# Optimization experiments

Measured on AMD Instinct MI355X. Metric: run time of the kernel, lower is better.

The kernel has to match this reference:

```python
import jax, jax.numpy as jnp
import numpy as np
import math

B, S, E, H = 8, 1024, 1024, 16
HD = E // H  # 64


def setup_inputs() -> dict:
    key = jax.random.key(0)
    ks = jax.random.split(key, 13)
    scale = 1.0 / math.sqrt(E)
    inp = {
        "query": jax.random.normal(ks[0], (B, S, E), jnp.float32),
        "key": jax.random.normal(ks[1], (B, S, E), jnp.float32),
        "value": jax.random.normal(ks[2], (B, S, E), jnp.float32),
        "mask": jax.random.randint(ks[3], (B, S, S), 0, 2, jnp.int32),
        "adjoin_matrix": jax.random.normal(ks[4], (B, S, S), jnp.float32),
        "Wq": jax.random.uniform(ks[5], (E, E), jnp.float32, -scale, scale),
        "bq": jax.random.uniform(ks[6], (E,), jnp.float32, -scale, scale),
        "Wk": jax.random.uniform(ks[7], (E, E), jnp.float32, -scale, scale),
        "bk": jax.random.uniform(ks[8], (E,), jnp.float32, -scale, scale),
        "Wv": jax.random.uniform(ks[9], (E, E), jnp.float32, -scale, scale),
        "bv": jax.random.uniform(ks[10], (E,), jnp.float32, -scale, scale),
        "Wo": jax.random.uniform(ks[11], (E, E), jnp.float32, -scale, scale),
        "bo": jax.random.uniform(ks[12], (E,), jnp.float32, -scale, scale),
    }
    return inp


def reference(query, key, value, mask, adjoin_matrix, Wq, bq, Wk, bk, Wv, bv, Wo, bo):
    def split_heads(x):
        # [B,S,E] -> [B,H,S,HD]
        return x.reshape(B, S, H, HD).transpose(0, 2, 1, 3)

    q = split_heads(query @ Wq.T + bq)
    k = split_heads(key @ Wk.T + bk)
    v = split_heads(value @ Wv.T + bv)

    # scaled logits: [B,H,S,S]
    logits = jnp.einsum("bhqd,bhkd->bhqk", q, k) / jnp.sqrt(jnp.asarray(HD, q.dtype))
    # additive mask (broadcast over heads)
    logits = logits + mask[:, None, :, :].astype(logits.dtype) * (-1e9)
    attn = jax.nn.softmax(logits, axis=-1)
    # post-softmax adjoin-matrix addition
    attn = attn + adjoin_matrix[:, None, :, :]

    x = jnp.einsum("bhqk,bhkd->bhqd", attn, v)  # [B,H,S,HD]
    x = x.transpose(0, 2, 1, 3).reshape(B, S, E)
    out = x @ Wo.T + bo
    return out, attn
```

## Files before the change

### kernel.cpp

```cpp
#include <hip/hip_runtime.h>
#include <stdint.h>

#define BB 8
#define SS 1024
#define EE 1024
#define HH 16
#define HDD 64

typedef unsigned short u16_t;
typedef __attribute__((ext_vector_type(8))) short short8;
typedef __attribute__((ext_vector_type(4))) float f32x4;

__device__ __forceinline__ u16_t f2bf(float f){
    union { float f; uint32_t u; } v; v.f = f;
    return (u16_t)((v.u + 0x7fffu + ((v.u >> 16) & 1u)) >> 16);
}
__device__ __forceinline__ float bf2f(u16_t u){
    union { uint32_t u; float f; } v; v.u = ((uint32_t)u) << 16;
    return v.f;
}

__device__ __forceinline__ void gload_lds16(const void* g, void* l){
    __builtin_amdgcn_global_load_lds((const __attribute__((address_space(1))) unsigned int*)g,
                                     (__attribute__((address_space(3))) unsigned int*)l, 16, 0, 0);
}

#define MFMA16(a,b,c) __builtin_amdgcn_mfma_f32_16x16x32_bf16(a,b,c,0,0,0)

union U8 { short8 v; u16_t u[8]; };

__global__ __launch_bounds__(256) void cvt3_f32_bf16(const float* __restrict__ s0,
                                                     const float* __restrict__ s1,
                                                     const float* __restrict__ s2,
                                                     u16_t* __restrict__ d0,
                                                     u16_t* __restrict__ d1,
                                                     u16_t* __restrict__ d2, int n8){
    const float* in = (blockIdx.z == 0) ? s0 : (blockIdx.z == 1 ? s1 : s2);
    u16_t* out      = (blockIdx.z == 0) ? d0 : (blockIdx.z == 1 ? d1 : d2);
    int i = blockIdx.x * blockDim.x + threadIdx.x;
    int stride = gridDim.x * blockDim.x;
    for (; i < n8; i += stride){
        const float4* p = (const float4*)(in + (size_t)i * 8);
        float4 a = p[0], b = p[1];
        U8 o;
        o.u[0]=f2bf(a.x); o.u[1]=f2bf(a.y); o.u[2]=f2bf(a.z); o.u[3]=f2bf(a.w);
        o.u[4]=f2bf(b.x); o.u[5]=f2bf(b.y); o.u[6]=f2bf(b.z); o.u[7]=f2bf(b.w);
        *(short8*)(out + (size_t)i * 8) = o.v;
    }
}

__global__ __launch_bounds__(256) void cvtW4_f32_bf16(const float* __restrict__ s0,
                                                      const float* __restrict__ s1,
                                                      const float* __restrict__ s2,
                                                      const float* __restrict__ s3,
                                                      u16_t* __restrict__ d0,
                                                      u16_t* __restrict__ d1,
                                                      u16_t* __restrict__ d2,
                                                      u16_t* __restrict__ d3, int n8){
    const float* in;
    u16_t* out;
    switch (blockIdx.z){
        case 0: in = s0; out = d0; break;
        case 1: in = s1; out = d1; break;
        case 2: in = s2; out = d2; break;
        default: in = s3; out = d3; break;
    }
    int i = blockIdx.x * blockDim.x + threadIdx.x;
    int stride = gridDim.x * blockDim.x;
    for (; i < n8; i += stride){
        const float4* p = (const float4*)(in + (size_t)i * 8);
        float4 a = p[0], b = p[1];
        U8 o;
        o.u[0]=f2bf(a.x); o.u[1]=f2bf(a.y); o.u[2]=f2bf(a.z); o.u[3]=f2bf(a.w);
        o.u[4]=f2bf(b.x); o.u[5]=f2bf(b.y); o.u[6]=f2bf(b.z); o.u[7]=f2bf(b.w);
        *(short8*)(out + (size_t)i * 8) = o.v;
    }
}

__global__ __launch_bounds__(256) void cvt_mask(const int* __restrict__ mask,
                                                u16_t* __restrict__ mb, int n8){
    int i = blockIdx.x * blockDim.x + threadIdx.x;
    int stride = gridDim.x * blockDim.x;
    for (; i < n8; i += stride){
        const int4* p = (const int4*)(mask + (size_t)i * 8);
        int4 a = p[0], b = p[1];
        U8 o;
        o.u[0]=a.x?0xCE6Eu:0u; o.u[1]=a.y?0xCE6Eu:0u; o.u[2]=a.z?0xCE6Eu:0u; o.u[3]=a.w?0xCE6Eu:0u;
        o.u[4]=b.x?0xCE6Eu:0u; o.u[5]=b.y?0xCE6Eu:0u; o.u[6]=b.z?0xCE6Eu:0u; o.u[7]=b.w?0xCE6Eu:0u;
        *(short8*)(mb + (size_t)i * 8) = o.v;
    }
}

__global__ __launch_bounds__(256) void transpose_v(const u16_t* __restrict__ Vp,
                                                   u16_t* __restrict__ Vt){
    __shared__ u16_t sT[64 * 66];
    const int b = blockIdx.z, h = blockIdx.y, s0 = blockIdx.x * 64;
    const int tid = threadIdx.x;
    #pragma unroll
    for (int it = 0; it < 2; it++){
        int c = it * 256 + tid;
        int sr = c >> 3, c8 = c & 7;
        short8 v = *(const short8*)(Vp + (size_t)(b * SS + s0 + sr) * EE + h * HDD + c8 * 8);
        *(short8*)(sT + sr * 66 + c8 * 8) = v;
    }
    __syncthreads();
    #pragma unroll
    for (int it = 0; it < 2; it++){
        int c = it * 256 + tid;
        int dr = c >> 3, c8 = c & 7;
        U8 o;
        #pragma unroll
        for (int e = 0; e < 8; e++) o.u[e] = sT[(c8 * 8 + e) * 66 + dr];
        *(short8*)(Vt + ((size_t)(b * HH + h) * HDD + dr) * SS + s0 + c8 * 8) = o.v;
    }
}

__device__ __forceinline__ void xcd_tiles(int& m0, int& n0){
    int i = blockIdx.x + blockIdx.y * 8;
    int k = i & 7, q = i >> 3;
    m0 = (k * 8 + (q >> 3)) * 128;
    n0 = (q & 7) * 128;
}

__global__ __launch_bounds__(256) void gemm_bt3(const u16_t* __restrict__ qb,
                                                const u16_t* __restrict__ kb,
                                                const u16_t* __restrict__ vb,
                                                const u16_t* __restrict__ Wqb,
                                                const u16_t* __restrict__ Wkb,
                                                const u16_t* __restrict__ Wvb,
                                                const float* __restrict__ bq,
                                                const float* __restrict__ bk,
                                                const float* __restrict__ bv,
                                                u16_t* __restrict__ Qp,
                                                u16_t* __restrict__ Kp,
                                                u16_t* __restrict__ Vp)
{
    const u16_t *A, *Bw; const float* bias; u16_t* Cout;
    switch (blockIdx.z){
        case 0:  A = qb; Bw = Wqb; bias = bq; Cout = Qp; break;
        case 1:  A = kb; Bw = Wkb; bias = bk; Cout = Kp; break;
        default: A = vb; Bw = Wvb; bias = bv; Cout = Vp; break;
    }
    const int K = EE, N = EE;

    __shared__ u16_t sA[128 * 32];
    __shared__ u16_t sB[128 * 32];
    const int tid = threadIdx.x;
    const int wave = tid >> 6, lane = tid & 63;
    int m0, n0; xcd_tiles(m0, n0);
    const int wm = (wave >> 1) * 64, wn = (wave & 1) * 64;

    f32x4 acc[4][4] = {};

    for (int k0 = 0; k0 < K; k0 += 32){
        #pragma unroll
        for (int i = 0; i < 2; i++){
            int s   = (wave * 2 + i) * 64 + lane;
            int row = s >> 2, cb = (s & 3) * 8;
            gload_lds16(A  + (size_t)(m0 + row) * K + k0 + cb, (void*)(sA + (wave * 2 + i) * 512));
            gload_lds16(Bw + (size_t)(n0 + row) * K + k0 + cb, (void*)(sB + (wave * 2 + i) * 512));
        }
        __syncthreads();

        short8 aF[4], bF[4];
        #pragma unroll
        for (int m = 0; m < 4; m++)
            aF[m] = *(const short8*)(sA + (wm + m * 16 + (lane & 15)) * 32 + (lane >> 4) * 8);
        #pragma unroll
        for (int n = 0; n < 4; n++)
            bF[n] = *(const short8*)(sB + (wn + n * 16 + (lane & 15)) * 32 + (lane >> 4) * 8);
        #pragma unroll
        for (int m = 0; m < 4; m++)
            #pragma unroll
            for (int n = 0; n < 4; n++)
                acc[m][n] = MFMA16(aF[m], bF[n], acc[m][n]);
        __syncthreads();
    }

    #pragma unroll
    for (int m = 0; m < 4; m++){
        #pragma unroll
        for (int n = 0; n < 4; n++){
            int col = n0 + wn + n * 16 + (lane & 15);
            float bvv = bias[col];
            #pragma unroll
            for (int j = 0; j < 4; j++){
                int row = m0 + wm + m * 16 + (lane >> 4) * 4 + j;
                Cout[(size_t)row * N + col] = f2bf(acc[m][n][j] + bvv);
            }
        }
    }
}

__global__ __launch_bounds__(256) void gemm_bt_f32(const u16_t* __restrict__ A,
                                                   const u16_t* __restrict__ Bw,
                                                   const float* __restrict__ bias,
                                                   float* __restrict__ Cout,
                                                   int M, int N, int K)
{
    __shared__ u16_t sA[128 * 32];
    __shared__ u16_t sB[128 * 32];
    const int tid = threadIdx.x;
    const int wave = tid >> 6, lane = tid & 63;
    int m0, n0; xcd_tiles(m0, n0);
    const int wm = (wave >> 1) * 64, wn = (wave & 1) * 64;

    f32x4 acc[4][4] = {};

    for (int k0 = 0; k0 < K; k0 += 32){
        #pragma unroll
        for (int i = 0; i < 2; i++){
            int s   = (wave * 2 + i) * 64 + lane;
            int row = s >> 2, cb = (s & 3) * 8;
            gload_lds16(A  + (size_t)(m0 + row) * K + k0 + cb, (void*)(sA + (wave * 2 + i) * 512));
            gload_lds16(Bw + (size_t)(n0 + row) * K + k0 + cb, (void*)(sB + (wave * 2 + i) * 512));
        }
        __syncthreads();

        short8 aF[4], bF[4];
        #pragma unroll
        for (int m = 0; m < 4; m++)
            aF[m] = *(const short8*)(sA + (wm + m * 16 + (lane & 15)) * 32 + (lane >> 4) * 8);
        #pragma unroll
        for (int n = 0; n < 4; n++)
            bF[n] = *(const short8*)(sB + (wn + n * 16 + (lane & 15)) * 32 + (lane >> 4) * 8);
        #pragma unroll
        for (int m = 0; m < 4; m++)
            #pragma unroll
            for (int n = 0; n < 4; n++)
                acc[m][n] = MFMA16(aF[m], bF[n], acc[m][n]);
        __syncthreads();
    }

    #pragma unroll
    for (int m = 0; m < 4; m++){
        #pragma unroll
        for (int n = 0; n < 4; n++){
            int col = n0 + wn + n * 16 + (lane & 15);
            float bv = bias[col];
            #pragma unroll
            for (int j = 0; j < 4; j++){
                int row = m0 + wm + m * 16 + (lane >> 4) * 4 + j;
                Cout[(size_t)row * N + col] = acc[m][n][j] + bv;
            }
        }
    }
}

__global__ __launch_bounds__(256, 3) void attn_fused(const u16_t* __restrict__ Qp,
                                                     const u16_t* __restrict__ Kp,
                                                     const u16_t* __restrict__ Vt,
                                                     const u16_t* __restrict__ maskb,
                                                     const float* __restrict__ adjoin,
                                                     float* __restrict__ attn,
                                                     u16_t* __restrict__ X)
{
    __shared__ u16_t sL[16384];
    u16_t* sVT = sL + 8192;
    u16_t* sPB = sL + 12288;

    const int flat = blockIdx.x;
    const int b  = flat & 7;
    const int i0 = ((flat >> 3) & 15) * 64;
    const int h  = flat >> 7;
    const int tid = threadIdx.x, wave = tid >> 6, lane = tid & 63;
    const int frow = lane & 15, fks = lane >> 4;
    const int bh = b * HH + h;

    #pragma unroll
    for (int i = 0; i < 2; i++){
        int chunk = (wave * 2 + i) * 64 + lane;
        int row = chunk >> 3, slot = chunk & 7;
        gload_lds16(Qp + (size_t)(b * SS + i0 + row) * EE + h * HDD + (slot ^ (row & 7)) * 8,
                    (void*)(sPB + (wave * 2 + i) * 512));
    }
    __syncthreads();
    short8 aQ0, aQ1;
    {
        int row = wave * 16 + frow;
        aQ0 = *(const short8*)((const char*)sPB + row * 128 + ((fks * 16)      ^ ((row & 7) << 4)));
        aQ1 = *(const short8*)((const char*)sPB + row * 128 + ((64 + fks * 16) ^ ((row & 7) << 4)));
    }
    __syncthreads();

    auto stageK64 = [&](int j0, u16_t* dst){
        #pragma unroll
        for (int i = 0; i < 2; i++){
            int chunk = (wave * 2 + i) * 64 + lane;
            int row = chunk >> 3, slot = chunk & 7;
            gload_lds16(Kp + (size_t)(b * SS + j0 + row) * EE + h * HDD + (slot ^ (row & 7)) * 8,
                        (void*)(dst + (wave * 2 + i) * 512));
        }
    };
    auto stageK128 = [&](int j0, u16_t* dst){
        #pragma unroll
        for (int i = 0; i < 4; i++){
            int chunk = (wave * 4 + i) * 64 + lane;
            int row = chunk >> 3, slot = chunk & 7;
            gload_lds16(Kp + (size_t)(b * SS + j0 + row) * EE + h * HDD + (slot ^ (row & 7)) * 8,
                        (void*)(dst + (wave * 4 + i) * 512));
        }
    };
    auto stageVT = [&](int j0){
        #pragma unroll
        for (int i = 0; i < 2; i++){
            int chunk = (wave * 2 + i) * 64 + lane;
            int row = chunk >> 3, slot = chunk & 7;
            gload_lds16(Vt + ((size_t)bh * HDD + row) * SS + j0 + (slot ^ (row & 7)) * 8,
                        (void*)(sVT + (wave * 2 + i) * 512));
        }
    };

    const int grow0 = i0 + wave * 16 + fks * 4;
    const size_t mrowbase = (size_t)(b * SS + grow0) * SS;

    float s_run[4] = {0.f, 0.f, 0.f, 0.f};
    {
        u16_t* bufs[2] = { sL, sL + 8192 };
        stageK128(0, bufs[0]);
        #pragma unroll
        for (int T = 0; T < 8; T++){
            u16_t* cur = bufs[T & 1];
            __syncthreads();
            if (T < 7) stageK128((T + 1) * 128, bufs[(T + 1) & 1]);
            #pragma unroll
            for (int half = 0; half < 2; half++){
                const int t64 = T * 128 + half * 64;
                float mbv[4][4];
                #pragma unroll
                for (int n = 0; n < 4; n++)
                    #pragma unroll
                    for (int r = 0; r < 4; r++)
                        mbv[n][r] = bf2f(maskb[mrowbase + (size_t)r * SS + t64 + n * 16 + frow]);
                __builtin_amdgcn_s_setprio(1);
                #pragma unroll
                for (int n = 0; n < 4; n++){
                    int jrow = half * 64 + n * 16 + frow;
                    f32x4 acc = {};
                    short8 bF = *(const short8*)((const char*)cur + jrow * 128 + ((fks * 16)      ^ ((jrow & 7) << 4)));
                    acc = MFMA16(aQ0, bF, acc);
                    bF        = *(const short8*)((const char*)cur + jrow * 128 + ((64 + fks * 16) ^ ((jrow & 7) << 4)));
                    acc = MFMA16(aQ1, bF, acc);
                    #pragma unroll
                    for (int r = 0; r < 4; r++)
                        s_run[r] += __expf(acc[r] * 0.125f + mbv[n][r]);
                }
                __builtin_amdgcn_s_setprio(0);
            }
        }
    }
    float inv[4];
    #pragma unroll
    for (int r = 0; r < 4; r++){
        float v = s_run[r];
        v += __shfl_xor(v, 1); v += __shfl_xor(v, 2); v += __shfl_xor(v, 4); v += __shfl_xor(v, 8);
        inv[r] = 1.0f / v;
    }

    f32x4 accPV[4] = {};
    __syncthreads();
    u16_t* sK2[2] = { sL, sL + 4096 };
    stageK64(0, sK2[0]);
    #pragma unroll
    for (int t = 0; t < 16; t++){
        const int cur = t & 1;
        __syncthreads();
        if (t < 15) stageK64((t + 1) * 64, sK2[cur ^ 1]);
        stageVT(t * 64);
        float mbv[4][4], adjv[4][4];
        #pragma unroll
        for (int n = 0; n < 4; n++)
            #pragma unroll
            for (int r = 0; r < 4; r++){
                size_t off = mrowbase + (size_t)r * SS + t * 64 + n * 16 + frow;
                mbv[n][r]  = bf2f(maskb[off]);
                adjv[n][r] = adjoin[off];
            }
        __builtin_amdgcn_s_setprio(1);
        #pragma unroll
        for (int n = 0; n < 4; n++){
            int jrow = n * 16 + frow;
            f32x4 acc = {};
            short8 bF = *(const short8*)((const char*)sK2[cur] + jrow * 128 + ((fks * 16)      ^ ((jrow & 7) << 4)));
            acc = MFMA16(aQ0, bF, acc);
            bF        = *(const short8*)((const char*)sK2[cur] + jrow * 128 + ((64 + fks * 16) ^ ((jrow & 7) << 4)));
            acc = MFMA16(aQ1, bF, acc);
            #pragma unroll
            for (int r = 0; r < 4; r++){
                int irow = wave * 16 + fks * 4 + r;
                float att = __expf(acc[r] * 0.125f + mbv[n][r]) * inv[r] + adjv[n][r];
                *(u16_t*)((char*)sPB + irow * 128 + (((n * 16 + frow) * 2) ^ ((irow & 7) << 4))) = f2bf(att);
            }
        }
        __builtin_amdgcn_s_setprio(0);
        __syncthreads();
        __builtin_amdgcn_s_setprio(1);
        {
            int prow = wave * 16 + frow;
            short8 aP0 = *(const short8*)((const char*)sPB + prow * 128 + ((fks * 16)      ^ ((prow & 7) << 4)));
            short8 aP1 = *(const short8*)((const char*)sPB + prow * 128 + ((64 + fks * 16) ^ ((prow & 7) << 4)));
            #pragma unroll
            for (int n = 0; n < 4; n++){
                int drow = n * 16 + frow;
                short8 bV0 = *(const short8*)((const char*)sVT + drow * 128 + ((fks * 16)      ^ ((drow & 7) << 4)));
                short8 bV1 = *(const short8*)((const char*)sVT + drow * 128 + ((64 + fks * 16) ^ ((drow & 7) << 4)));
                accPV[n] = MFMA16(aP0, bV0, accPV[n]);
                accPV[n] = MFMA16(aP1, bV1, accPV[n]);
            }
        }
        __builtin_amdgcn_s_setprio(0);
        {
            int rr = tid >> 4, c4 = tid & 15;
            #pragma unroll
            for (int it = 0; it < 4; it++){
                int row = it * 16 + rr;
                uint2 pv = *(const uint2*)((const char*)sPB + row * 128 + ((c4 * 8) ^ ((row & 7) << 4)));
                float4 o;
                o.x = bf2f((u16_t)(pv.x & 0xffffu));
                o.y = bf2f((u16_t)(pv.x >> 16));
                o.z = bf2f((u16_t)(pv.y & 0xffffu));
                o.w = bf2f((u16_t)(pv.y >> 16));
                *(float4*)(attn + ((size_t)bh * SS + i0 + row) * SS + t * 64 + c4 * 4) = o;
            }
        }
    }

    #pragma unroll
    for (int n = 0; n < 4; n++){
        #pragma unroll
        for (int j = 0; j < 4; j++){
            int row = i0 + wave * 16 + fks * 4 + j;
            int col = h * HDD + n * 16 + frow;
            X[(size_t)(b * SS + row) * EE + col] = f2bf(accPV[n][j]);
        }
    }
}

extern "C" void kernel_launch(void* const* d_in, const int* in_sizes, int n_in,
                              void* d_out, int out_size, void* d_ws, size_t ws_size,
                              hipStream_t stream)
{
    const float* query  = (const float*)d_in[0];
    const float* key    = (const float*)d_in[1];
    const float* value  = (const float*)d_in[2];
    const int*   mask   = (const int*)  d_in[3];
    const float* adjoin = (const float*)d_in[4];
    const float* Wq = (const float*)d_in[5];
    const float* bq = (const float*)d_in[6];
    const float* Wk = (const float*)d_in[7];
    const float* bk = (const float*)d_in[8];
    const float* Wv = (const float*)d_in[9];
    const float* bv = (const float*)d_in[10];
    const float* Wo = (const float*)d_in[11];
    const float* bo = (const float*)d_in[12];

    float* out  = (float*)d_out;
    float* attn = out + (size_t)BB * SS * EE;

    const size_t nBSE = (size_t)BB * SS * EE;
    const size_t nEE  = (size_t)EE * EE;

    u16_t* p  = (u16_t*)d_ws;
    u16_t* qb  = p; p += nBSE;
    u16_t* kb  = p; p += nBSE;
    u16_t* vb  = p; p += nBSE;
    u16_t* Qp  = p; p += nBSE;
    u16_t* Kp  = p; p += nBSE;
    u16_t* Vp  = p; p += nBSE;
    u16_t* Xa  = p; p += nBSE;
    u16_t* Wqb = p; p += nEE;
    u16_t* Wkb = p; p += nEE;
    u16_t* Wvb = p; p += nEE;
    u16_t* Wob = p; p += nEE;

    u16_t* Vt    = qb;
    u16_t* maskb = kb;

    cvt3_f32_bf16<<<dim3(1024, 1, 3), 256, 0, stream>>>(query, key, value, qb, kb, vb, (int)(nBSE / 8));
    cvtW4_f32_bf16<<<dim3(256, 1, 4), 256, 0, stream>>>(Wq, Wk, Wv, Wo, Wqb, Wkb, Wvb, Wob, (int)(nEE / 8));

    dim3 gProj(EE / 128, (BB * SS) / 128);
    gemm_bt3<<<dim3(EE / 128, (BB * SS) / 128, 3), 256, 0, stream>>>(qb, kb, vb, Wqb, Wkb, Wvb,
                                                                     bq, bk, bv, Qp, Kp, Vp);

    dim3 gT(SS / 64, HH, BB);
    transpose_v<<<gT, 256, 0, stream>>>(Vp, Vt);
    cvt_mask<<<1024, 256, 0, stream>>>(mask, maskb, (int)(nBSE / 8));

    attn_fused<<<2048, 256, 0, stream>>>(Qp, Kp, Vt, maskb, adjoin, attn, Xa);

    gemm_bt_f32<<<gProj, 256, 0, stream>>>(Xa, Wob, bo, out, BB * SS, EE, EE);
}
```

Measured before the change: 406.7 us.

## Process 128 keys per barrier pair in attention second pass

Restructures the second attention pass so each iteration handles two 64-key halves, with separate K, V-transpose and probability buffers for each half. This halves the number of block-wide barriers and loop iterations, amortising synchronisation cost. K is no longer double-buffered across iterations; the next K tile is issued after the barrier instead of prefetched earlier. Shared memory grows from 32KB to 48KB, which may limit occupancy at the declared 3 blocks per CU.

```diff
diff --git a/kernel.cpp b/kernel.cpp
--- a/kernel.cpp
+++ b/kernel.cpp
@@ -255,9 +255,13 @@
                                                      float* __restrict__ attn,
                                                      u16_t* __restrict__ X)
 {
-    __shared__ u16_t sL[16384];
-    u16_t* sVT = sL + 8192;
-    u16_t* sPB = sL + 12288;
+    __shared__ u16_t sL[24576];
+    u16_t* sK0  = sL;
+    u16_t* sK1  = sL + 4096;
+    u16_t* sVT0 = sL + 8192;
+    u16_t* sVT1 = sL + 12288;
+    u16_t* sPB0 = sL + 16384;
+    u16_t* sPB1 = sL + 20480;
 
     const int flat = blockIdx.x;
     const int b  = flat & 7;
@@ -272,14 +276,14 @@
         int chunk = (wave * 2 + i) * 64 + lane;
         int row = chunk >> 3, slot = chunk & 7;
         gload_lds16(Qp + (size_t)(b * SS + i0 + row) * EE + h * HDD + (slot ^ (row & 7)) * 8,
-                    (void*)(sPB + (wave * 2 + i) * 512));
+                    (void*)(sPB0 + (wave * 2 + i) * 512));
     }
     __syncthreads();
     short8 aQ0, aQ1;
     {
         int row = wave * 16 + frow;
-        aQ0 = *(const short8*)((const char*)sPB + row * 128 + ((fks * 16)      ^ ((row & 7) << 4)));
-        aQ1 = *(const short8*)((const char*)sPB + row * 128 + ((64 + fks * 16) ^ ((row & 7) << 4)));
+        aQ0 = *(const short8*)((const char*)sPB0 + row * 128 + ((fks * 16)      ^ ((row & 7) << 4)));
+        aQ1 = *(const short8*)((const char*)sPB0 + row * 128 + ((64 + fks * 16) ^ ((row & 7) << 4)));
     }
     __syncthreads();
 
@@ -301,13 +305,13 @@
                         (void*)(dst + (wave * 4 + i) * 512));
         }
     };
-    auto stageVT = [&](int j0){
+    auto stageVT64 = [&](int j0, u16_t* dst){
         #pragma unroll
         for (int i = 0; i < 2; i++){
             int chunk = (wave * 2 + i) * 64 + lane;
             int row = chunk >> 3, slot = chunk & 7;
             gload_lds16(Vt + ((size_t)bh * HDD + row) * SS + j0 + (slot ^ (row & 7)) * 8,
-                        (void*)(sVT + (wave * 2 + i) * 512));
+                        (void*)(dst + (wave * 2 + i) * 512));
         }
     };
 
@@ -359,68 +363,78 @@
 
     f32x4 accPV[4] = {};
     __syncthreads();
-    u16_t* sK2[2] = { sL, sL + 4096 };
-    stageK64(0, sK2[0]);
-    #pragma unroll
-    for (int t = 0; t < 16; t++){
-        const int cur = t & 1;
+    stageK64(0, sK0); stageK64(64, sK1);
+    #pragma unroll
+    for (int T = 0; T < 8; T++){
         __syncthreads();
-        if (t < 15) stageK64((t + 1) * 64, sK2[cur ^ 1]);
-        stageVT(t * 64);
-        float mbv[4][4], adjv[4][4];
-        #pragma unroll
-        for (int n = 0; n < 4; n++)
-            #pragma unroll
-            for (int r = 0; r < 4; r++){
-                size_t off = mrowbase + (size_t)r * SS + t * 64 + n * 16 + frow;
-                mbv[n][r]  = bf2f(maskb[off]);
-                adjv[n][r] = adjoin[off];
+        stageVT64(T * 128, sVT0);
+        stageVT64(T * 128 + 64, sVT1);
+        #pragma unroll
+        for (int half = 0; half < 2; half++){
+            const u16_t* sKh = half ? sK1 : sK0;
+            u16_t* sPh = half ? sPB1 : sPB0;
+            const int t64 = T * 128 + half * 64;
+            float mbv[4][4], adjv[4][4];
+            #pragma unroll
+            for (int n = 0; n < 4; n++)
+                #pragma unroll
+                for (int r = 0; r < 4; r++){
+                    size_t off = mrowbase + (size_t)r * SS + t64 + n * 16 + frow;
+                    mbv[n][r]  = bf2f(maskb[off]);
+                    adjv[n][r] = adjoin[off];
+                }
+            __builtin_amdgcn_s_setprio(1);
+            #pragma unroll
+            for (int n = 0; n < 4; n++){
+                int jrow = n * 16 + frow;
+                f32x4 acc = {};
+                short8 bF = *(const short8*)((const char*)sKh + jrow * 128 + ((fks * 16)      ^ ((jrow & 7) << 4)));
+                acc = MFMA16(aQ0, bF, acc);
+                bF        = *(const short8*)((const char*)sKh + jrow * 128 + ((64 + fks * 16) ^ ((jrow & 7) << 4)));
+                acc = MFMA16(aQ1, bF, acc);
+                #pragma unroll
+                for (int r = 0; r < 4; r++){
+                    int irow = wave * 16 + fks * 4 + r;
+                    float att = __expf(acc[r] * 0.125f + mbv[n][r]) * inv[r] + adjv[n][r];
+                    *(u16_t*)((char*)sPh + irow * 128 + (((n * 16 + frow) * 2) ^ ((irow & 7) << 4))) = f2bf(att);
+                }
             }
+            __builtin_amdgcn_s_setprio(0);
+        }
+        __syncthreads();
+        if (T < 7){ stageK64((T + 1) * 128, sK0); stageK64((T + 1) * 128 + 64, sK1); }
         __builtin_amdgcn_s_setprio(1);
         #pragma unroll
-        for (int n = 0; n < 4; n++){
-            int jrow = n * 16 + frow;
-            f32x4 acc = {};
-            short8 bF = *(const short8*)((const char*)sK2[cur] + jrow * 128 + ((fks * 16)      ^ ((jrow & 7) << 4)));
-            acc = MFMA16(aQ0, bF, acc);
-            bF        = *(const short8*)((const char*)sK2[cur] + jrow * 128 + ((64 + fks * 16) ^ ((jrow & 7) << 4)));
-            acc = MFMA16(aQ1, bF, acc);
-            #pragma unroll
-            for (int r = 0; r < 4; r++){
-                int irow = wave * 16 + fks * 4 + r;
-                float att = __expf(acc[r] * 0.125f + mbv[n][r]) * inv[r] + adjv[n][r];
-                *(u16_t*)((char*)sPB + irow * 128 + (((n * 16 + frow) * 2) ^ ((irow & 7) << 4))) = f2bf(att);
-            }
-        }
-        __builtin_amdgcn_s_setprio(0);
-        __syncthreads();
-        __builtin_amdgcn_s_setprio(1);
-        {
+        for (int half = 0; half < 2; half++){
+            const u16_t* sVh = half ? sVT1 : sVT0;
+            const u16_t* sPh = half ? sPB1 : sPB0;
             int prow = wave * 16 + frow;
-            short8 aP0 = *(const short8*)((const char*)sPB + prow * 128 + ((fks * 16)      ^ ((prow & 7) << 4)));
-            short8 aP1 = *(const short8*)((const char*)sPB + prow * 128 + ((64 + fks * 16) ^ ((prow & 7) << 4)));
+            short8 aP0 = *(const short8*)((const char*)sPh + prow * 128 + ((fks * 16)      ^ ((prow & 7) << 4)));
+            short8 aP1 = *(const short8*)((const char*)sPh + prow * 128 + ((64 + fks * 16) ^ ((prow & 7) << 4)));
             #pragma unroll
             for (int n = 0; n < 4; n++){
                 int drow = n * 16 + frow;
-                short8 bV0 = *(const short8*)((const char*)sVT + drow * 128 + ((fks * 16)      ^ ((drow & 7) << 4)));
-                short8 bV1 = *(const short8*)((const char*)sVT + drow * 128 + ((64 + fks * 16) ^ ((drow & 7) << 4)));
+                short8 bV0 = *(const short8*)((const char*)sVh + drow * 128 + ((fks * 16)      ^ ((drow & 7) << 4)));
+                short8 bV1 = *(const short8*)((const char*)sVh + drow * 128 + ((64 + fks * 16) ^ ((drow & 7) << 4)));
                 accPV[n] = MFMA16(aP0, bV0, accPV[n]);
                 accPV[n] = MFMA16(aP1, bV1, accPV[n]);
             }
         }
         __builtin_amdgcn_s_setprio(0);
-        {
+        #pragma unroll
+        for (int half = 0; half < 2; half++){
+            const u16_t* sPh = half ? sPB1 : sPB0;
             int rr = tid >> 4, c4 = tid & 15;
             #pragma unroll
             for (int it = 0; it < 4; it++){
                 int row = it * 16 + rr;
-                uint2 pv = *(const uint2*)((const char*)sPB + row * 128 + ((c4 * 8) ^ ((row & 7) << 4)));
+                uint2 pv = *(const uint2*)((const char*)sPh + row * 128 + ((c4 * 8) ^ ((row & 7) << 4)));
                 float4 o;
                 o.x = bf2f((u16_t)(pv.x & 0xffffu));
                 o.y = bf2f((u16_t)(pv.x >> 16));
                 o.z = bf2f((u16_t)(pv.y & 0xffffu));
                 o.w = bf2f((u16_t)(pv.y >> 16));
-                *(float4*)(attn + ((size_t)bh * SS + i0 + row) * SS + t * 64 + c4 * 4) = o;
+                *(float4*)(attn + ((size_t)bh * SS + i0 + row) * SS + T * 128 + half * 64 + c4 * 4) = o;
             }
         }
     }
```

After: 397.8 us. -2.2%, faster.
